# Optimization experiments

Hardware: AMD Instinct MI355X
Metric: run time of the kernel (lower is better)

Reference implementation:

```python
import jax, jax.numpy as jnp
import numpy as np

# neuralef_loss_cfg constants
T = 10.0
K_FEAT = 32           # num_nearestn_feature
K_PIX1 = 10           # num_nearestn_pixel1 (distance_weight 2.0)
K_PIX2 = 10           # num_nearestn_pixel2 (distance_weight 0.1)
PIXELWISE_WEIGHT = 1.0
ALPHA = 0.05
NO_SG = False


def setup_inputs() -> dict:
    key = jax.random.key(0)
    k1, k2, k3 = jax.random.split(key, 3)
    bs, n, d = 8, 1024, 768
    h = w = 32  # token grid; bs*h*w == Psi rows
    kpsi = 512
    highlevel_feature = jax.random.normal(k1, (bs, n, d), jnp.float32)
    Psi = jax.random.normal(k2, (bs * n, kpsi), jnp.float32)
    im = jax.random.uniform(k3, (bs, 3, h, w), jnp.float32, minval=-1.0, maxval=1.0)
    return {"highlevel_feature": highlevel_feature, "Psi": Psi, "im": im}


def _build_graphs(highlevel_feature, im):
    # --- feature kNN affinity over all bs*n tokens ---
    bs, n, d = highlevel_feature.shape
    N = bs * n
    f = highlevel_feature.reshape(N, d)
    f = f / jnp.linalg.norm(f, axis=-1, keepdims=True)
    A = f @ f.T
    # torch: diag<- -inf then clamp(min=0) => diag becomes 0, negatives clipped
    A = jnp.clip(A, 0.0)
    A = A.at[jnp.arange(N), jnp.arange(N)].set(0.0)
    vals, idx = jax.lax.top_k(A, K_FEAT)
    res = jnp.zeros_like(A).at[jnp.arange(N)[:, None], idx].set(vals)
    A = (res + res.T) * 0.5

    # --- pixel kNN graph per image (color + weighted coords) ---
    im01 = (im + 1.0) * 0.5
    h, w = im.shape[2], im.shape[3]
    hw = h * w
    x_ = jnp.tile(jnp.linspace(0.0, 1.0, w), (h,)).reshape(1, hw, 1)
    y_ = jnp.repeat(jnp.linspace(0.0, 1.0, h), w).reshape(1, hw, 1)
    pix = im01.reshape(bs, 3, hw).transpose(0, 2, 1)  # [bs, hw, 3]
    eye = jnp.eye(hw, dtype=bool)[None]
    A_p = jnp.zeros((bs, hw, hw), dtype=bool)
    for k, dw in zip([K_PIX1, K_PIX2], [2.0, 0.1]):
        if k == 0:
            continue
        im2 = jnp.concatenate(
            [pix,
             jnp.broadcast_to(x_ * dw, (bs, hw, 1)),
             jnp.broadcast_to(y_ * dw, (bs, hw, 1))], axis=-1)
        sq = jnp.sum(im2 * im2, axis=-1)  # [bs, hw]
        d2 = sq[:, :, None] + sq[:, None, :] - 2.0 * jnp.einsum('bnc,bmc->bnm', im2, im2)
        euc = -jnp.sqrt(jnp.maximum(d2, 0.0))
        euc = jnp.where(eye, -jnp.inf, euc)
        _, pidx = jax.lax.top_k(euc, k)
        resb = jnp.zeros((bs, hw, hw), dtype=bool).at[
            jnp.arange(bs)[:, None, None],
            jnp.arange(hw)[None, :, None],
            pidx].set(True)
        A_p = A_p | resb | resb.transpose(0, 2, 1)

    A2 = jax.scipy.linalg.block_diag(*A_p.astype(jnp.float32))  # [N, N]

    D = 1.0 / jnp.sqrt(A.sum(-1))
    G1 = A * D[None, :] * D[:, None]
    D2 = 1.0 / jnp.sqrt(A2.sum(-1))
    G2 = A2 * D2[None, :] * D2[:, None]
    return G1, G2


def _neuralef_loss(Psi, G1, G2):
    N, K = Psi.shape
    Psi = Psi * jnp.sqrt(T / N)
    Psi1, Psi2 = jnp.split(Psi, 2, axis=-1)
    loss = 0.0
    reg = 0.0
    for P, G, wt in [(Psi1, G1, 1.0), (Psi2, G2, PIXELWISE_WEIGHT)]:
        GP = G @ P                   # [N, K/2]
        R = P.T @ GP                 # [K/2, K/2]
        R_hat = R if NO_SG else jax.lax.stop_gradient(P).T @ GP
        loss = loss + (-jnp.trace(R) / K) * wt
        reg = reg + (jnp.sum(jnp.triu(R_hat ** 2, 1)) / K) * wt
    return loss, reg * ALPHA


def reference(highlevel_feature, Psi, im):
    # graph construction is under torch.no_grad in the original
    G1, G2 = jax.lax.stop_gradient(_build_graphs(highlevel_feature, im))
    return _neuralef_loss(Psi, G1, G2)
```

## Files before the change

### kernel.cpp

```cpp
#include <hip/hip_runtime.h>
#include <hip/hip_bf16.h>
#include <cstdint>
#include <cstddef>

#define NTOK 8192
#define DFEAT 768
#define HW 1024
#define BSZ 8
#define KPSI 512
#define KH 256
#define KF 32
#define KPIX 10
#define NB2 128
#define CANDCAP 128
#define BM2 256
#define BK 64
#define SROWS 2048
#define SJCAP 160

typedef __attribute__((ext_vector_type(8))) short bf16x8_t;
typedef __attribute__((ext_vector_type(4))) float f32x4;

__device__ __forceinline__ bool gt_pair(float va, int ia, float vb, int ib) {
  return (va > vb) || (va == vb && ia < ib);
}
__device__ __forceinline__ bool lt_pair(float va, int ia, float vb, int ib) {
  return (va < vb) || (va == vb && ia < ib);
}

__device__ __forceinline__ void gload_lds16(const void* g, void* l) {
  __builtin_amdgcn_global_load_lds((const __attribute__((address_space(1))) void*)g,
                                   (__attribute__((address_space(3))) void*)l, 16, 0, 0);
}

__global__ __launch_bounds__(256) void ksplit(const float* __restrict__ X,
                                              __hip_bfloat16* __restrict__ Y) {
  int row = blockIdx.x;
  int tid = threadIdx.x;
  const float* x = X + (size_t)row * DFEAT;
  float s = 0.f;
  for (int c = tid; c < DFEAT; c += 256) { float v = x[c]; s += v * v; }
  __shared__ float red[4];
  #pragma unroll
  for (int o = 32; o > 0; o >>= 1) s += __shfl_down(s, o);
  if ((tid & 63) == 0) red[tid >> 6] = s;
  __syncthreads();
  if (tid == 0) red[0] = red[0] + red[1] + red[2] + red[3];
  __syncthreads();
  float nrm = sqrtf(red[0]);
  __hip_bfloat16* y = Y + (size_t)row * (2 * DFEAT);
  for (int c = tid; c < DFEAT; c += 256) {
    float v = x[c] / nrm;
    __hip_bfloat16 hi = __float2bfloat16(v);
    __hip_bfloat16 lo = __float2bfloat16(v - __bfloat162float(hi));
    y[c] = hi;
    y[DFEAT + c] = lo;
  }
}

__global__ __launch_bounds__(256) void kpixfeat(const float* __restrict__ im,
                                                float* __restrict__ pf) {
  int t = blockIdx.x * 256 + threadIdx.x;
  int img = t >> 10, p = t & 1023;
  float r = (im[((size_t)img * 3 + 0) * HW + p] + 1.0f) * 0.5f;
  float g = (im[((size_t)img * 3 + 1) * HW + p] + 1.0f) * 0.5f;
  float b = (im[((size_t)img * 3 + 2) * HW + p] + 1.0f) * 0.5f;
  float x = (float)(p & 31) * (1.0f / 31.0f);
  float y = (float)(p >> 5) * (1.0f / 31.0f);
  #pragma unroll
  for (int cfg = 0; cfg < 2; cfg++) {
    float dw = cfg ? 0.1f : 2.0f;
    float xx = x * dw, yy = y * dw;
    float sq = r * r + g * g + b * b + xx * xx + yy * yy;
    float* o = pf + (((size_t)cfg * BSZ + img) * HW + p) * 6;
    o[0] = r; o[1] = g; o[2] = b; o[3] = xx; o[4] = yy; o[5] = sq;
  }
}

__global__ __launch_bounds__(256) void kpixtopk(const float* __restrict__ pf,
                                                unsigned int* __restrict__ bits) {
  int wglobal = blockIdx.x * 4 + (threadIdx.x >> 6);
  int lane = threadIdx.x & 63;
  int cfg = wglobal & 1;
  int gr = wglobal >> 1;
  int img = gr >> 10, i = gr & 1023;
  const float* base = pf + ((size_t)cfg * BSZ + img) * HW * 6;
  const float* fi = base + (size_t)i * 6;
  float r = fi[0], g = fi[1], b = fi[2], x = fi[3], y = fi[4], sq = fi[5];
  float d[16];
  #pragma unroll
  for (int q = 0; q < 16; q++) {
    int j = q * 64 + lane;
    const float* fj = base + (size_t)j * 6;
    float dot = r * fj[0] + g * fj[1] + b * fj[2] + x * fj[3] + y * fj[4];
    float d2 = fmaxf(sq + fj[5] - 2.0f * dot, 0.0f);
    d[q] = (j == i) ? 3.402823e38f : d2;
  }
  for (int k = 0; k < KPIX; k++) {
    float bv = 3.402823e38f; int bj = 1 << 30;
    #pragma unroll
    for (int q = 0; q < 16; q++) {
      int j = q * 64 + lane;
      if (lt_pair(d[q], j, bv, bj)) { bv = d[q]; bj = j; }
    }
    #pragma unroll
    for (int o = 32; o > 0; o >>= 1) {
      float ov = __shfl_down(bv, o); int oj = __shfl_down(bj, o);
      if (lt_pair(ov, oj, bv, bj)) { bv = ov; bj = oj; }
    }
    bj = __shfl(bj, 0);
    if ((bj & 63) == lane) d[bj >> 6] = 3.402823e38f;
    if (lane == 0) {
      atomicOr(&bits[((size_t)img * HW + i) * 32 + (bj >> 5)], 1u << (bj & 31));
      atomicOr(&bits[((size_t)img * HW + bj) * 32 + (i >> 5)], 1u << (i & 31));
    }
  }
}

__global__ __launch_bounds__(256) void kdeg2(const unsigned int* __restrict__ bits,
                                             float* __restrict__ d2n) {
  int i = blockIdx.x * 256 + threadIdx.x;
  int c = 0;
  #pragma unroll
  for (int w = 0; w < 32; w++) c += __popc(bits[(size_t)i * 32 + w]);
  d2n[i] = 1.0f / sqrtf((float)c);
}

__global__ __launch_bounds__(1024) void kgemm256(const __hip_bfloat16* __restrict__ X,
                                                 float* __restrict__ C,
                                                 int row0, int nwg) {
  __shared__ __hip_bfloat16 sA[2][BM2 * BK];
  __shared__ __hip_bfloat16 sB[2][BM2 * BK];
  int cpx = nwg >> 3;
  int flat = blockIdx.x;
  int swz = (flat & 7) * cpx + (flat >> 3);
  int by = swz >> 5, bx = swz & 31;
  int tid = threadIdx.x;
  int wid = tid >> 6, lane = tid & 63;
  int wr = wid >> 2, wc = wid & 3;
  int l15 = lane & 15, l4 = lane >> 4, l7 = lane & 7;
  int srow = tid >> 3, sc = tid & 7;

  f32x4 acc[4][4];
  #pragma unroll
  for (int m = 0; m < 4; m++)
    #pragma unroll
    for (int n = 0; n < 4; n++) acc[m][n] = (f32x4){0.f, 0.f, 0.f, 0.f};

  const size_t arow0 = (size_t)(row0 + by * BM2);
  const size_t brow0 = (size_t)(bx * BM2);

  auto stage = [&](int ks, int buf) {
    int s = ks / 12;
    int k0 = (ks - s * 12) * 64;
    int aoff = (s == 2) ? DFEAT : 0;
    int boff = (s == 1) ? DFEAT : 0;
    #pragma unroll
    for (int i = 0; i < 2; i++) {
      int row = i * 128 + srow;
      int gcol = (sc ^ (row & 7)) * 8;
      gload_lds16(X + (arow0 + row) * (2 * DFEAT) + aoff + k0 + gcol,
                  &sA[buf][(size_t)i * 8192 + (tid & ~63) * 8]);
      gload_lds16(X + (brow0 + row) * (2 * DFEAT) + boff + k0 + gcol,
                  &sB[buf][(size_t)i * 8192 + (tid & ~63) * 8]);
    }
  };

  stage(0, 0);
  stage(1, 1);
  for (int ks = 0; ks < 36; ks++) {
    int cur = ks & 1;
    if (ks < 35) { asm volatile("s_waitcnt vmcnt(4)" ::: "memory"); }
    else         { asm volatile("s_waitcnt vmcnt(0)" ::: "memory"); }
    __builtin_amdgcn_sched_barrier(0);
    __builtin_amdgcn_s_barrier();
    __builtin_amdgcn_sched_barrier(0);
    const char* Ab = (const char*)&sA[cur][0];
    const char* Bb = (const char*)&sB[cur][0];
    #pragma unroll
    for (int kk = 0; kk < 2; kk++) {
      bf16x8_t a[4], b[4];
      int chunk = (l4 + kk * 4) ^ l7;
      #pragma unroll
      for (int m = 0; m < 4; m++) {
        int rowa = wr * 64 + m * 16 + l15;
        a[m] = *(const bf16x8_t*)(Ab + rowa * 128 + chunk * 16);
      }
      #pragma unroll
      for (int n = 0; n < 4; n++) {
        int rowb = wc * 64 + n * 16 + l15;
        b[n] = *(const bf16x8_t*)(Bb + rowb * 128 + chunk * 16);
      }
      __builtin_amdgcn_s_setprio(1);
      #pragma unroll
      for (int m = 0; m < 4; m++)
        #pragma unroll
        for (int n = 0; n < 4; n++)
          acc[m][n] = __builtin_amdgcn_mfma_f32_16x16x32_bf16(a[m], b[n], acc[m][n], 0, 0, 0);
      __builtin_amdgcn_s_setprio(0);
    }
    __builtin_amdgcn_sched_barrier(0);
    __builtin_amdgcn_s_barrier();
    __builtin_amdgcn_sched_barrier(0);
    if (ks + 2 < 36) stage(ks + 2, cur);
  }
  #pragma unroll
  for (int m = 0; m < 4; m++)
    #pragma unroll
    for (int j = 0; j < 4; j++) {
      int crow = by * BM2 + wr * 64 + m * 16 + l4 * 4 + j;
      float* cp = C + (size_t)crow * NTOK + bx * BM2 + wc * 64 + l15;
      #pragma unroll
      for (int n = 0; n < 4; n++) cp[n * 16] = acc[m][n][j];
    }
}

__global__ __launch_bounds__(256) void ktopkf(const float* __restrict__ Astrip, int row0,
                                              float* __restrict__ tvo, int* __restrict__ tio) {
  const int r = blockIdx.x, row = row0 + r, tid = threadIdx.x;
  __shared__ int hist4[4][NB2];
  __shared__ int suf[NB2];
  __shared__ float cv[CANDCAP];
  __shared__ int   ci[CANDCAP];
  __shared__ int ncnt;
  __shared__ int tsh;
  const int wave = tid >> 6;
  const float* arow = Astrip + (size_t)r * NTOK;
  for (int b = tid; b < 4 * NB2; b += 256) ((int*)hist4)[b] = 0;
  if (tid == 0) ncnt = 0;
  __syncthreads();
  float4 v4s[8];
  #pragma unroll
  for (int q = 0; q < 8; q++) {
    int c = (q * 256 + tid) * 4;
    float4 v4 = *(const float4*)(arow + c);
    v4s[q] = v4;
    float vv[4] = {v4.x, v4.y, v4.z, v4.w};
    #pragma unroll
    for (int e = 0; e < 4; e++) {
      float v = vv[e];
      if (v > 0.0f && (c + e) != row) {
        int b = (int)(__float_as_uint(v) >> 19) - 1920;
        if (b >= 0) atomicAdd(&hist4[wave][b], 1);
      }
    }
  }
  __syncthreads();
  if (tid < NB2) suf[tid] = hist4[0][tid] + hist4[1][tid] + hist4[2][tid] + hist4[3][tid];
  __syncthreads();
  for (int o = 1; o < NB2; o <<= 1) {
    int v = (tid < NB2 && tid + o < NB2) ? suf[tid + o] : 0;
    __syncthreads();
    if (tid < NB2) suf[tid] += v;
    __syncthreads();
  }
  if (tid < NB2) {
    int tail = (tid + 1 < NB2) ? suf[tid + 1] : 0;
    if (suf[tid] >= KF && tail < KF) tsh = 1920 + tid;
  }
  if (tid == 0 && suf[0] < KF) tsh = 1;
  __syncthreads();
  int t = tsh;
  #pragma unroll
  for (int q = 0; q < 8; q++) {
    int c = (q * 256 + tid) * 4;
    float vv[4] = {v4s[q].x, v4s[q].y, v4s[q].z, v4s[q].w};
    #pragma unroll
    for (int e = 0; e < 4; e++) {
      float v = vv[e];
      if (v > 0.0f && (c + e) != row && (int)(__float_as_uint(v) >> 19) >= t) {
        int p = atomicAdd(&ncnt, 1);
        if (p < CANDCAP) { cv[p] = v; ci[p] = c + e; }
      }
    }
  }
  __syncthreads();
  int nc = ncnt < CANDCAP ? ncnt : CANDCAP;
  if (tid < nc) {
    float v = cv[tid]; int idx = ci[tid];
    int rank = 0;
    for (int j = 0; j < nc; j++)
      if (gt_pair(cv[j], ci[j], v, idx)) rank++;
    if (rank < KF) {
      tvo[(size_t)row * KF + rank] = v;
      tio[(size_t)row * KF + rank] = idx;
    }
  }
  int wrote = nc < KF ? nc : KF;
  for (int k = wrote + tid; k < KF; k += 256) {
    tvo[(size_t)row * KF + k] = 0.0f;
    tio[(size_t)row * KF + k] = -1;
  }
}

__global__ __launch_bounds__(256) void kcnt(const int* __restrict__ tio,
                                            int* __restrict__ cnt) {
  int t = blockIdx.x * 256 + threadIdx.x;
  int j = tio[t];
  if (j >= 0) {
    int i = t >> 5;
    atomicAdd(&cnt[i], 1);
    atomicAdd(&cnt[j], 1);
  }
}

__global__ __launch_bounds__(1024) void kscan(const int* __restrict__ cnt,
                                              int* __restrict__ offs,
                                              int* __restrict__ cur) {
  __shared__ int part[1024];
  int tid = threadIdx.x;
  int base = tid * 8;
  int loc[8]; int s = 0;
  #pragma unroll
  for (int q = 0; q < 8; q++) { loc[q] = s; s += cnt[base + q]; }
  part[tid] = s;
  __syncthreads();
  for (int o = 1; o < 1024; o <<= 1) {
    int v = 0;
    if (tid >= o) v = part[tid - o];
    __syncthreads();
    if (tid >= o) part[tid] += v;
    __syncthreads();
  }
  int pre = (tid == 0) ? 0 : part[tid - 1];
  #pragma unroll
  for (int q = 0; q < 8; q++) { offs[base + q] = pre + loc[q]; cur[base + q] = pre + loc[q]; }
  if (tid == 1023) offs[NTOK] = part[1023];
}

__global__ __launch_bounds__(256) void kscat(const float* __restrict__ tvo,
                                             const int* __restrict__ tio,
                                             int* __restrict__ cur,
                                             int* __restrict__ colA,
                                             float* __restrict__ valA) {
  int t = blockIdx.x * 256 + threadIdx.x;
  int j = tio[t];
  if (j >= 0) {
    int i = t >> 5;
    float v = tvo[t] * 0.5f;
    int p = atomicAdd(&cur[i], 1); colA[p] = j; valA[p] = v;
    int q = atomicAdd(&cur[j], 1); colA[q] = i; valA[q] = v;
  }
}

__global__ __launch_bounds__(256) void kdeg1(const int* __restrict__ offs,
                                             const float* __restrict__ valA,
                                             float* __restrict__ d1) {
  int i = blockIdx.x * 256 + threadIdx.x;
  float s = 0.f;
  int e0 = offs[i], e1 = offs[i + 1];
  for (int e = e0; e < e1; e++) s += valA[e];
  d1[i] = 1.0f / sqrtf(s);
}

__global__ __launch_bounds__(256) void kprescale(const int* __restrict__ offs,
                                                 const int* __restrict__ colA,
                                                 const float* __restrict__ d1,
                                                 float* __restrict__ valA) {
  int i = blockIdx.x * 4 + (threadIdx.x >> 6);
  int lane = threadIdx.x & 63;
  float di = d1[i];
  int e0 = offs[i], e1 = offs[i + 1];
  for (int e = e0 + lane; e < e1; e += 64) valA[e] *= di * d1[colA[e]];
}

__global__ __launch_bounds__(256) void kspmm1(const int* __restrict__ offs,
                                              const int* __restrict__ colA,
                                              const float* __restrict__ valA,
                                              const float* __restrict__ Psi,
                                              float* __restrict__ GP1) {
  int i = blockIdx.x;
  int c = threadIdx.x;
  __shared__ int   sj[128];
  __shared__ float sw[128];
  float acc = 0.f;
  int e0 = offs[i], e1 = offs[i + 1];
  for (int base = e0; base < e1; base += 128) {
    int nb = e1 - base; if (nb > 128) nb = 128;
    __syncthreads();
    if (c < nb) { sj[c] = colA[base + c]; sw[c] = valA[base + c]; }
    __syncthreads();
    int e = 0;
    for (; e + 8 <= nb; e += 8) {
      float p0 = Psi[(size_t)sj[e + 0] * KPSI + c];
      float p1 = Psi[(size_t)sj[e + 1] * KPSI + c];
      float p2 = Psi[(size_t)sj[e + 2] * KPSI + c];
      float p3 = Psi[(size_t)sj[e + 3] * KPSI + c];
      float p4 = Psi[(size_t)sj[e + 4] * KPSI + c];
      float p5 = Psi[(size_t)sj[e + 5] * KPSI + c];
      float p6 = Psi[(size_t)sj[e + 6] * KPSI + c];
      float p7 = Psi[(size_t)sj[e + 7] * KPSI + c];
      acc += sw[e + 0] * p0; acc += sw[e + 1] * p1;
      acc += sw[e + 2] * p2; acc += sw[e + 3] * p3;
      acc += sw[e + 4] * p4; acc += sw[e + 5] * p5;
      acc += sw[e + 6] * p6; acc += sw[e + 7] * p7;
    }
    for (; e + 4 <= nb; e += 4) {
      float p0 = Psi[(size_t)sj[e + 0] * KPSI + c];
      float p1 = Psi[(size_t)sj[e + 1] * KPSI + c];
      float p2 = Psi[(size_t)sj[e + 2] * KPSI + c];
      float p3 = Psi[(size_t)sj[e + 3] * KPSI + c];
      acc += sw[e + 0] * p0; acc += sw[e + 1] * p1;
      acc += sw[e + 2] * p2; acc += sw[e + 3] * p3;
    }
    for (; e < nb; e++) acc += sw[e] * Psi[(size_t)sj[e] * KPSI + c];
  }
  GP1[(size_t)i * KH + c] = acc;
}

__global__ __launch_bounds__(256) void kspmm2(const unsigned int* __restrict__ bits,
                                              const float* __restrict__ d2n,
                                              const float* __restrict__ Psi,
                                              float* __restrict__ GP2) {
  int i = blockIdx.x;
  int base = (i >> 10) << 10;
  int c = threadIdx.x;
  __shared__ int   sj[SJCAP];
  __shared__ float sw[SJCAP];
  __shared__ int scnt;
  if (c < 32) {
    unsigned int w = bits[(size_t)i * 32 + c];
    int n = __popc(w);
    int pre = n;
    #pragma unroll
    for (int o = 1; o < 32; o <<= 1) {
      int v = __shfl_up(pre, o);
      if (c >= o) pre += v;
    }
    pre -= n;
    int k = pre;
    while (w) {
      int b = __ffs(w) - 1; w &= w - 1;
      int j = base + c * 32 + b;
      if (k < SJCAP) { sj[k] = j; sw[k] = d2n[j]; }
      k++;
    }
    if (c == 31) scnt = pre + n;
  }
  __syncthreads();
  int nb = scnt; if (nb > SJCAP) nb = SJCAP;
  float acc = 0.f;
  int e = 0;
  for (; e + 8 <= nb; e += 8) {
    float p0 = Psi[(size_t)sj[e + 0] * KPSI + KH + c];
    float p1 = Psi[(size_t)sj[e + 1] * KPSI + KH + c];
    float p2 = Psi[(size_t)sj[e + 2] * KPSI + KH + c];
    float p3 = Psi[(size_t)sj[e + 3] * KPSI + KH + c];
    float p4 = Psi[(size_t)sj[e + 4] * KPSI + KH + c];
    float p5 = Psi[(size_t)sj[e + 5] * KPSI + KH + c];
    float p6 = Psi[(size_t)sj[e + 6] * KPSI + KH + c];
    float p7 = Psi[(size_t)sj[e + 7] * KPSI + KH + c];
    acc += sw[e + 0] * p0; acc += sw[e + 1] * p1;
    acc += sw[e + 2] * p2; acc += sw[e + 3] * p3;
    acc += sw[e + 4] * p4; acc += sw[e + 5] * p5;
    acc += sw[e + 6] * p6; acc += sw[e + 7] * p7;
  }
  for (; e + 4 <= nb; e += 4) {
    float p0 = Psi[(size_t)sj[e + 0] * KPSI + KH + c];
    float p1 = Psi[(size_t)sj[e + 1] * KPSI + KH + c];
    float p2 = Psi[(size_t)sj[e + 2] * KPSI + KH + c];
    float p3 = Psi[(size_t)sj[e + 3] * KPSI + KH + c];
    acc += sw[e + 0] * p0; acc += sw[e + 1] * p1;
    acc += sw[e + 2] * p2; acc += sw[e + 3] * p3;
  }
  for (; e < nb; e++) acc += sw[e] * Psi[(size_t)sj[e] * KPSI + KH + c];
  GP2[(size_t)i * KH + c] = acc * d2n[i];
}

__global__ __launch_bounds__(256) void kR(const float* __restrict__ Psi,
                                          const float* __restrict__ GP1,
                                          const float* __restrict__ GP2,
                                          float* __restrict__ R) {
  static const int tmap[10] = {0,0,0,0,1,1,1,2,2,3};
  static const int nmap[10] = {0,1,2,3,1,2,3,2,3,3};
  int g = blockIdx.z;
  const float* GP = g ? GP2 : GP1;
  int colOff = g ? KH : 0;
  int tile = blockIdx.x;
  int tm0 = tmap[tile] * 64, tn0 = nmap[tile] * 64;
  int k0 = blockIdx.y * 256;
  __shared__ float As2[16][68];
  __shared__ float Bs2[16][68];
  int tid = threadIdx.x;
  int tx = tid & 15, ty = tid >> 4;
  int lkk = tid >> 4, lq = (tid & 15) * 4;
  float acc[4][4] = {};
  for (int kk0 = 0; kk0 < 256; kk0 += 16) {
    int krow = k0 + kk0 + lkk;
    float4 a = *(const float4*)&Psi[(size_t)krow * KPSI + colOff + tm0 + lq];
    float4 b = *(const float4*)&GP[(size_t)krow * KH + tn0 + lq];
    As2[lkk][lq + 0] = a.x; As2[lkk][lq + 1] = a.y; As2[lkk][lq + 2] = a.z; As2[lkk][lq + 3] = a.w;
    Bs2[lkk][lq + 0] = b.x; Bs2[lkk][lq + 1] = b.y; Bs2[lkk][lq + 2] = b.z; Bs2[lkk][lq + 3] = b.w;
    __syncthreads();
    #pragma unroll
    for (int k = 0; k < 16; k++) {
      const float4 av = *(const float4*)&As2[k][ty * 4];
      const float4 bv = *(const float4*)&Bs2[k][tx * 4];
      float aa[4] = {av.x, av.y, av.z, av.w};
      float bb[4] = {bv.x, bv.y, bv.z, bv.w};
      #pragma unroll
      for (int i2 = 0; i2 < 4; i2++)
        #pragma unroll
        for (int j2 = 0; j2 < 4; j2++)
          acc[i2][j2] += aa[i2] * bb[j2];
    }
    __syncthreads();
  }
  #pragma unroll
  for (int i2 = 0; i2 < 4; i2++)
    #pragma unroll
    for (int j2 = 0; j2 < 4; j2++)
      atomicAdd(&R[(size_t)g * KH * KH + (size_t)(tm0 + ty * 4 + i2) * KH + tn0 + tx * 4 + j2],
                acc[i2][j2]);
}

__global__ __launch_bounds__(256) void kfinal1(const float* __restrict__ R,
                                               double* __restrict__ part) {
  const double s2 = 10.0 / 8192.0;
  int blk = blockIdx.x, tid = threadIdx.x;
  double tr = 0.0, rg = 0.0;
  #pragma unroll
  for (int q = 0; q < 4; q++) {
    int t = blk * 1024 + q * 256 + tid;
    int t2 = t & 65535;
    int i = t2 >> 8, j = t2 & 255;
    double v = (double)R[t] * s2;
    if (i == j) tr += v;
    else if (j > i) rg += v * v;
  }
  __shared__ double sa[4], sb[4];
  #pragma unroll
  for (int o = 32; o > 0; o >>= 1) { tr += __shfl_down(tr, o); rg += __shfl_down(rg, o); }
  if ((tid & 63) == 0) { sa[tid >> 6] = tr; sb[tid >> 6] = rg; }
  __syncthreads();
  if (tid == 0) {
    part[blk * 2 + 0] = sa[0] + sa[1] + sa[2] + sa[3];
    part[blk * 2 + 1] = sb[0] + sb[1] + sb[2] + sb[3];
  }
}

__global__ __launch_bounds__(128) void kfinal2(const double* __restrict__ part,
                                               float* __restrict__ out) {
  int tid = threadIdx.x;
  double tr = part[tid * 2 + 0];
  double rg = part[tid * 2 + 1];
  __shared__ double sa[2], sb[2];
  #pragma unroll
  for (int o = 32; o > 0; o >>= 1) { tr += __shfl_down(tr, o); rg += __shfl_down(rg, o); }
  if ((tid & 63) == 0) { sa[tid >> 6] = tr; sb[tid >> 6] = rg; }
  __syncthreads();
  if (tid == 0) {
    tr = sa[0] + sa[1];
    rg = sb[0] + sb[1];
    out[0] = (float)(-tr / 512.0);
    out[1] = (float)((rg / 512.0) * 0.05);
  }
}

extern "C" void kernel_launch(void* const* d_in, const int* in_sizes, int n_in,
                              void* d_out, int out_size, void* d_ws, size_t ws_size,
                              hipStream_t stream) {
  const float* hf  = (const float*)d_in[0];
  const float* Psi = (const float*)d_in[1];
  const float* im  = (const float*)d_in[2];
  float* out = (float*)d_out;

  char* base = (char*)d_ws;
  size_t off = 0;
  auto alloc = [&](size_t bytes) -> void* {
    void* p = base + off;
    off += (bytes + 255) & ~(size_t)255;
    return p;
  };

  __hip_bfloat16* Xs = (__hip_bfloat16*)alloc((size_t)NTOK * 2 * DFEAT * 2);
  float* tv    = (float*)alloc((size_t)NTOK * KF * 4);
  int*   ti    = (int*)  alloc((size_t)NTOK * KF * 4);
  int*   cnt   = (int*)  alloc((size_t)NTOK * 4);
  int*   offs  = (int*)  alloc((size_t)(NTOK + 1) * 4);
  int*   cur   = (int*)  alloc((size_t)NTOK * 4);
  int*   colA  = (int*)  alloc((size_t)NTOK * KF * 2 * 4);
  float* valA  = (float*)alloc((size_t)NTOK * KF * 2 * 4);
  float* d1    = (float*)alloc((size_t)NTOK * 4);
  float* GP1   = (float*)alloc((size_t)NTOK * KH * 4);
  float* GP2   = (float*)alloc((size_t)NTOK * KH * 4);
  unsigned int* bits = (unsigned int*)alloc((size_t)NTOK * 32 * 4);
  float* d2n   = (float*)alloc((size_t)NTOK * 4);
  float* pf    = (float*)alloc((size_t)2 * BSZ * HW * 6 * 4);
  float* Rm    = (float*)alloc((size_t)2 * KH * KH * 4);
  double* partd = (double*)alloc((size_t)128 * 2 * 8);
  float* Astrip = (float*)(base + off);

  size_t rem = (ws_size > off) ? (ws_size - off) : 0;
  long srows = (long)(rem / ((size_t)NTOK * 4));
  srows &= ~255L;
  if (srows < 256) srows = 256;
  if (srows > SROWS) srows = SROWS;

  hipMemsetAsync(cnt, 0, (size_t)NTOK * 4, stream);
  hipMemsetAsync(bits, 0, (size_t)NTOK * 32 * 4, stream);
  hipMemsetAsync(Rm, 0, (size_t)2 * KH * KH * 4, stream);

  ksplit<<<NTOK, 256, 0, stream>>>(hf, Xs);
  kpixfeat<<<(BSZ * HW) / 256, 256, 0, stream>>>(im, pf);
  kpixtopk<<<(BSZ * HW * 2) / 4, 256, 0, stream>>>(pf, bits);
  kdeg2<<<NTOK / 256, 256, 0, stream>>>(bits, d2n);

  for (int row0 = 0; row0 < NTOK; row0 += (int)srows) {
    int rows = NTOK - row0;
    if (rows > srows) rows = (int)srows;
    int nwg = (rows / BM2) * (NTOK / BM2);
    kgemm256<<<nwg, 1024, 0, stream>>>(Xs, Astrip, row0, nwg);
    ktopkf<<<rows, 256, 0, stream>>>(Astrip, row0, tv, ti);
  }

  kcnt<<<(NTOK * KF) / 256, 256, 0, stream>>>(ti, cnt);
  kscan<<<1, 1024, 0, stream>>>(cnt, offs, cur);
  kscat<<<(NTOK * KF) / 256, 256, 0, stream>>>(tv, ti, cur, colA, valA);
  kdeg1<<<NTOK / 256, 256, 0, stream>>>(offs, valA, d1);
  kprescale<<<NTOK / 4, 256, 0, stream>>>(offs, colA, d1, valA);
  kspmm1<<<NTOK, 256, 0, stream>>>(offs, colA, valA, Psi, GP1);
  kspmm2<<<NTOK, 256, 0, stream>>>(bits, d2n, Psi, GP2);
  kR<<<dim3(10, 32, 2), 256, 0, stream>>>(Psi, GP1, GP2, Rm);
  kfinal1<<<128, 256, 0, stream>>>(Rm, partd);
  kfinal2<<<1, 128, 0, stream>>>(partd, out);
}
```

Baseline: 704.9 us.

## Process top-k rows one per wavefront and pad pixel features to float4

The feature top-k kernel now assigns one row per 64-lane wave (four rows per block) instead of one row per 256-thread block. Block-wide __syncthreads and the LDS suffix scan are replaced by wave-local fences and shuffle-based scans. The row is read from global memory twice instead of being held in registers, which adds memory traffic but removes block barriers. Separately, pixel features are padded from 6 to 8 floats so the pixel kNN kernel can use float4 loads.

Measured after the change: 800.2 us. 1.14x slower.

```diff
diff --git a/kernel.cpp b/kernel.cpp
--- a/kernel.cpp
+++ b/kernel.cpp
@@ -33,6 +33,11 @@
                                    (__attribute__((address_space(3))) void*)l, 16, 0, 0);
 }
 
+__device__ __forceinline__ void wave_fence_lds() {
+  asm volatile("s_waitcnt lgkmcnt(0)" ::: "memory");
+  __builtin_amdgcn_wave_barrier();
+}
+
 __global__ __launch_bounds__(256) void ksplit(const float* __restrict__ X,
                                               __hip_bfloat16* __restrict__ Y) {
   int row = blockIdx.x;
@@ -72,8 +77,9 @@
     float dw = cfg ? 0.1f : 2.0f;
     float xx = x * dw, yy = y * dw;
     float sq = r * r + g * g + b * b + xx * xx + yy * yy;
-    float* o = pf + (((size_t)cfg * BSZ + img) * HW + p) * 6;
-    o[0] = r; o[1] = g; o[2] = b; o[3] = xx; o[4] = yy; o[5] = sq;
+    float* o = pf + (((size_t)cfg * BSZ + img) * HW + p) * 8;
+    *(float4*)(o)     = make_float4(r, g, b, xx);
+    *(float4*)(o + 4) = make_float4(yy, sq, 0.f, 0.f);
   }
 }
 
@@ -84,16 +90,18 @@
   int cfg = wglobal & 1;
   int gr = wglobal >> 1;
   int img = gr >> 10, i = gr & 1023;
-  const float* base = pf + ((size_t)cfg * BSZ + img) * HW * 6;
-  const float* fi = base + (size_t)i * 6;
-  float r = fi[0], g = fi[1], b = fi[2], x = fi[3], y = fi[4], sq = fi[5];
+  const float* base = pf + ((size_t)cfg * BSZ + img) * HW * 8;
+  float4 fa = *(const float4*)(base + (size_t)i * 8);
+  float4 fb = *(const float4*)(base + (size_t)i * 8 + 4);
+  float r = fa.x, g = fa.y, b = fa.z, x = fa.w, y = fb.x, sq = fb.y;
   float d[16];
   #pragma unroll
   for (int q = 0; q < 16; q++) {
     int j = q * 64 + lane;
-    const float* fj = base + (size_t)j * 6;
-    float dot = r * fj[0] + g * fj[1] + b * fj[2] + x * fj[3] + y * fj[4];
-    float d2 = fmaxf(sq + fj[5] - 2.0f * dot, 0.0f);
+    float4 ja = *(const float4*)(base + (size_t)j * 8);
+    float4 jb = *(const float4*)(base + (size_t)j * 8 + 4);
+    float dot = r * ja.x + g * ja.y + b * ja.z + x * ja.w + y * jb.x;
+    float d2 = fmaxf(sq + jb.y - 2.0f * dot, 0.0f);
     d[q] = (j == i) ? 3.402823e38f : d2;
   }
   for (int k = 0; k < KPIX; k++) {
@@ -217,77 +225,80 @@
 
 __global__ __launch_bounds__(256) void ktopkf(const float* __restrict__ Astrip, int row0,
                                               float* __restrict__ tvo, int* __restrict__ tio) {
-  const int r = blockIdx.x, row = row0 + r, tid = threadIdx.x;
-  __shared__ int hist4[4][NB2];
-  __shared__ int suf[NB2];
-  __shared__ float cv[CANDCAP];
-  __shared__ int   ci[CANDCAP];
-  __shared__ int ncnt;
-  __shared__ int tsh;
-  const int wave = tid >> 6;
+  const int wv = threadIdx.x >> 6, lane = threadIdx.x & 63;
+  const int r = blockIdx.x * 4 + wv, row = row0 + r;
+  __shared__ int   hist[4][NB2];
+  __shared__ float cv[4][CANDCAP];
+  __shared__ int   ci[4][CANDCAP];
+  __shared__ int   ncnt[4];
   const float* arow = Astrip + (size_t)r * NTOK;
-  for (int b = tid; b < 4 * NB2; b += 256) ((int*)hist4)[b] = 0;
-  if (tid == 0) ncnt = 0;
-  __syncthreads();
-  float4 v4s[8];
-  #pragma unroll
-  for (int q = 0; q < 8; q++) {
-    int c = (q * 256 + tid) * 4;
+  hist[wv][lane] = 0; hist[wv][lane + 64] = 0;
+  if (lane == 0) ncnt[wv] = 0;
+  wave_fence_lds();
+  for (int q = 0; q < 32; q++) {
+    int c = (q * 64 + lane) * 4;
     float4 v4 = *(const float4*)(arow + c);
-    v4s[q] = v4;
     float vv[4] = {v4.x, v4.y, v4.z, v4.w};
     #pragma unroll
     for (int e = 0; e < 4; e++) {
       float v = vv[e];
       if (v > 0.0f && (c + e) != row) {
         int b = (int)(__float_as_uint(v) >> 19) - 1920;
-        if (b >= 0) atomicAdd(&hist4[wave][b], 1);
+        if (b >= 0) atomicAdd(&hist[wv][b], 1);
       }
     }
   }
-  __syncthreads();
-  if (tid < NB2) suf[tid] = hist4[0][tid] + hist4[1][tid] + hist4[2][tid] + hist4[3][tid];
-  __syncthreads();
-  for (int o = 1; o < NB2; o <<= 1) {
-    int v = (tid < NB2 && tid + o < NB2) ? suf[tid + o] : 0;
-    __syncthreads();
-    if (tid < NB2) suf[tid] += v;
-    __syncthreads();
-  }
-  if (tid < NB2) {
-    int tail = (tid + 1 < NB2) ? suf[tid + 1] : 0;
-    if (suf[tid] >= KF && tail < KF) tsh = 1920 + tid;
-  }
-  if (tid == 0 && suf[0] < KF) tsh = 1;
-  __syncthreads();
-  int t = tsh;
-  #pragma unroll
-  for (int q = 0; q < 8; q++) {
-    int c = (q * 256 + tid) * 4;
-    float vv[4] = {v4s[q].x, v4s[q].y, v4s[q].z, v4s[q].w};
+  wave_fence_lds();
+  int h0 = hist[wv][2 * lane], h1 = hist[wv][2 * lane + 1];
+  int s = h0 + h1;
+  #pragma unroll
+  for (int o = 1; o < 64; o <<= 1) {
+    int t2 = __shfl_down(s, o);
+    if (lane + o < 64) s += t2;
+  }
+  int sNext = __shfl_down(s, 1);
+  if (lane == 63) sNext = 0;
+  int tb = -1;
+  if ((sNext + h1 >= KF) && (sNext < KF)) tb = 2 * lane + 1;
+  else if ((s >= KF) && (sNext + h1 < KF)) tb = 2 * lane;
+  #pragma unroll
+  for (int o = 32; o > 0; o >>= 1) {
+    int ot = __shfl_down(tb, o);
+    if (ot > tb) tb = ot;
+  }
+  tb = __shfl(tb, 0);
+  int t = (tb < 0) ? 1 : 1920 + tb;
+  for (int q = 0; q < 32; q++) {
+    int c = (q * 64 + lane) * 4;
+    float4 v4 = *(const float4*)(arow + c);
+    float vv[4] = {v4.x, v4.y, v4.z, v4.w};
     #pragma unroll
     for (int e = 0; e < 4; e++) {
       float v = vv[e];
       if (v > 0.0f && (c + e) != row && (int)(__float_as_uint(v) >> 19) >= t) {
-        int p = atomicAdd(&ncnt, 1);
-        if (p < CANDCAP) { cv[p] = v; ci[p] = c + e; }
+        int p = atomicAdd(&ncnt[wv], 1);
+        if (p < CANDCAP) { cv[wv][p] = v; ci[wv][p] = c + e; }
       }
     }
   }
-  __syncthreads();
-  int nc = ncnt < CANDCAP ? ncnt : CANDCAP;
-  if (tid < nc) {
-    float v = cv[tid]; int idx = ci[tid];
-    int rank = 0;
-    for (int j = 0; j < nc; j++)
-      if (gt_pair(cv[j], ci[j], v, idx)) rank++;
-    if (rank < KF) {
-      tvo[(size_t)row * KF + rank] = v;
-      tio[(size_t)row * KF + rank] = idx;
+  wave_fence_lds();
+  int nc = ncnt[wv]; if (nc > CANDCAP) nc = CANDCAP;
+  #pragma unroll
+  for (int h = 0; h < 2; h++) {
+    int cidx = h * 64 + lane;
+    if (cidx < nc) {
+      float v = cv[wv][cidx]; int idx = ci[wv][cidx];
+      int rank = 0;
+      for (int j = 0; j < nc; j++)
+        if (gt_pair(cv[wv][j], ci[wv][j], v, idx)) rank++;
+      if (rank < KF) {
+        tvo[(size_t)row * KF + rank] = v;
+        tio[(size_t)row * KF + rank] = idx;
+      }
     }
   }
   int wrote = nc < KF ? nc : KF;
-  for (int k = wrote + tid; k < KF; k += 256) {
+  for (int k = wrote + lane; k < KF; k += 64) {
     tvo[(size_t)row * KF + k] = 0.0f;
     tio[(size_t)row * KF + k] = -1;
   }
@@ -586,7 +597,7 @@
   float* GP2   = (float*)alloc((size_t)NTOK * KH * 4);
   unsigned int* bits = (unsigned int*)alloc((size_t)NTOK * 32 * 4);
   float* d2n   = (float*)alloc((size_t)NTOK * 4);
-  float* pf    = (float*)alloc((size_t)2 * BSZ * HW * 6 * 4);
+  float* pf    = (float*)alloc((size_t)2 * BSZ * HW * 8 * 4);
   float* Rm    = (float*)alloc((size_t)2 * KH * KH * 4);
   double* partd = (double*)alloc((size_t)128 * 2 * 8);
   float* Astrip = (float*)(base + off);
@@ -611,7 +622,7 @@
     if (rows > srows) rows = (int)srows;
     int nwg = (rows / BM2) * (NTOK / BM2);
     kgemm256<<<nwg, 1024, 0, stream>>>(Xs, Astrip, row0, nwg);
-    ktopkf<<<rows, 256, 0, stream>>>(Astrip, row0, tv, ti);
+    ktopkf<<<rows / 4, 256, 0, stream>>>(Astrip, row0, tv, ti);
   }
 
   kcnt<<<(NTOK * KF) / 256, 256, 0, stream>>>(ti, cnt);
```
